# Optimization experiments

Hardware: AMD Instinct MI355X
Metric: run time of the kernel (lower is better)

## Reference

```python
import jax, jax.numpy as jnp
import numpy as np

BETA = 0.25
DECAY = 0.99
USAGE_DECAY = 0.99
EPS = 1e-5
RESET_THRESHOLD = 100.0


def _sqdist(x, e):
    # squared euclidean distances [N, K]; argmin identical to cdist argmin
    x2 = jnp.sum(x * x, axis=1, keepdims=True)           # [N,1]
    e2 = jnp.sum(e * e, axis=1)[None, :]                 # [1,K]
    return x2 - 2.0 * (x @ e.T) + e2


def setup_inputs() -> dict:
    key = jax.random.key(0)
    ks = jax.random.split(key, 7)
    N, K, D = 32768, 4096, 256
    return {
        "x": jax.random.normal(ks[0], (N, D), jnp.float32),
        "embedding": jax.random.normal(ks[1], (K, D), jnp.float32) * (1.0 / K),
        "ema_cluster_size": jax.random.uniform(ks[2], (K,), jnp.float32),
        "ema_w": jax.random.normal(ks[3], (K, D), jnp.float32) * (1.0 / K),
        "codebook_usage": jax.random.uniform(ks[4], (K,), jnp.float32),
        "steps_since_used": jax.random.randint(ks[5], (K,), 0, 200, jnp.int32),
        "random_indices": jax.random.randint(ks[6], (K,), 0, N, jnp.int32),
    }


def reference(x, embedding, ema_cluster_size, ema_w, codebook_usage,
              steps_since_used, random_indices):
    N, D = x.shape
    K = embedding.shape[0]

    # --- nearest-code lookup ---
    d2 = _sqdist(x, embedding)                 # [N,K]
    indices = jnp.argmin(d2, axis=1)           # [N]
    q = jnp.take(embedding, indices, axis=0)   # [N,D]
    quantized = x + jax.lax.stop_gradient(q - x)

    commitment_loss = jnp.mean((x - jax.lax.stop_gradient(quantized)) ** 2)
    loss = BETA * commitment_loss

    # --- EMA codebook update (encodings.sum(0) and encodings.T @ x as segment sums) ---
    counts = jax.ops.segment_sum(jnp.ones((N,), x.dtype), indices, num_segments=K)
    dw = jax.ops.segment_sum(x, indices, num_segments=K)        # [K,D]
    new_cs = ema_cluster_size * DECAY + (1.0 - DECAY) * counts
    new_ema_w = ema_w * DECAY + (1.0 - DECAY) * dw
    n = jnp.sum(new_cs)
    cluster_size = (new_cs + EPS) / (n + K * EPS) * n
    new_embedding = new_ema_w / cluster_size[:, None]
    new_usage = codebook_usage * USAGE_DECAY + (1.0 - USAGE_DECAY) * counts

    # --- dead-code reset (uses the EMA-updated codebook, as in the original) ---
    idx2 = jnp.argmin(_sqdist(x, new_embedding), axis=1)
    used = jax.ops.segment_sum(jnp.ones((N,), x.dtype), idx2, num_segments=K) > 0
    steps = jnp.where(used, 0.0, steps_since_used.astype(x.dtype) + 1.0)
    dead = steps > RESET_THRESHOLD
    replacement = jnp.take(x, random_indices, axis=0)           # [K,D]
    new_embedding = jnp.where(dead[:, None], replacement, new_embedding)
    steps = jnp.where(dead, 0.0, steps)

    usage_rate = jnp.mean((new_usage > 0).astype(x.dtype))

    return (quantized, indices, loss, new_embedding, new_cs, new_ema_w,
            new_usage, steps, usage_rate)
```

## Files before the change

### kernel.cpp

```cpp
#include <hip/hip_runtime.h>
#include <math.h>

typedef float vf4 __attribute__((ext_vector_type(4)));
typedef _Float16 f16;
typedef _Float16 f16x8 __attribute__((ext_vector_type(8)));
typedef _Float16 f16x4 __attribute__((ext_vector_type(4)));
typedef float f32x4 __attribute__((ext_vector_type(4)));

static constexpr int Ncnt = 32768;
static constexpr int Kcb  = 4096;
static constexpr int Dim  = 256;

static constexpr float EPSf  = 1e-5f;
static constexpr float KEPSf = (float)(4096.0 * 1e-5);

static constexpr size_t OQ  = 0;
static constexpr size_t OI  = (size_t)Ncnt * Dim;
static constexpr size_t OL  = OI + Ncnt;
static constexpr size_t OE  = OL + 1;
static constexpr size_t OCS = OE + (size_t)Kcb * Dim;
static constexpr size_t OW  = OCS + Kcb;
static constexpr size_t OU  = OW + (size_t)Kcb * Dim;
static constexpr size_t OS  = OU + Kcb;
static constexpr size_t OR  = OS + Kcb;

__device__ __forceinline__ float np_sq256(const float* __restrict__ p) {
  float tot[2];
  #pragma unroll
  for (int h = 0; h < 2; ++h) {
    const float* a = p + h * 128;
    float r[8];
    #pragma unroll
    for (int j = 0; j < 8; ++j) r[j] = __fmul_rn(a[j], a[j]);
    for (int i = 8; i < 128; i += 8)
      #pragma unroll
      for (int j = 0; j < 8; ++j) r[j] = __fadd_rn(r[j], __fmul_rn(a[i + j], a[i + j]));
    tot[h] = __fadd_rn(__fadd_rn(__fadd_rn(r[0], r[1]), __fadd_rn(r[2], r[3])),
                       __fadd_rn(__fadd_rn(r[4], r[5]), __fadd_rn(r[6], r[7])));
  }
  return __fadd_rn(tot[0], tot[1]);
}

__global__ void rowsq_np(const float* __restrict__ E, float* __restrict__ e2, int rows) {
  const int k = blockIdx.x * 256 + threadIdx.x;
  if (k < rows) e2[k] = np_sq256(E + (size_t)k * Dim);
}

__global__ void split_rows(const float* __restrict__ src, f16* __restrict__ dst,
                           const float scale, const int rows)
{
  const int i   = blockIdx.x * 256 + threadIdx.x;
  const int row = i >> 6;
  const int d0  = (i & 63) * 4;
  if (row >= rows) return;
  const vf4 v = *(const vf4*)(src + (size_t)row * 256 + d0);
  f16x4 hi, lo;
  #pragma unroll
  for (int j = 0; j < 4; ++j) {
    const float t = __fmul_rn(v[j], scale);
    const f16 h   = (f16)t;
    const float r = __fsub_rn(t, (float)h);
    hi[j] = h;
    lo[j] = (f16)r;
  }
  *(f16x4*)(dst + (size_t)row * 512 + d0)       = hi;
  *(f16x4*)(dst + (size_t)row * 512 + 256 + d0) = lo;
}

__global__ __launch_bounds__(256, 2) void mfma_argmin(
    const f16* __restrict__ Xs, const f16* __restrict__ Es,
    const float* __restrict__ e2, const float two_scale,
    int* __restrict__ cand)
{
  __shared__ __align__(16) f16 As[128 * 32];
  __shared__ __align__(16) f16 Bs[128 * 32];

  const int tid  = threadIdx.x;
  const int bid  = blockIdx.x;
  const int row0 = (bid >> 3) * 128;
  const int cg   = bid & 7;
  const int colbase = cg * 512;

  const int lane = tid & 63;
  const int wv   = tid >> 6;
  const int wr   = wv >> 1;
  const int wc   = wv & 1;
  const int lc   = lane & 15;
  const int kc   = lane >> 4;

  const int sr  = tid >> 1;
  const int sh  = tid & 1;
  const int ssw = (sr >> 1) & 3;
  f16* lA = As + sr * 32;
  f16* lB = Bs + sr * 32;
  const int w0 = ((2 * sh)     ^ ssw) * 8;
  const int w1 = ((2 * sh + 1) ^ ssw) * 8;

  const f16* aG = Xs + (size_t)(row0 + sr) * 512 + sh * 16;

  const int ks = (kc ^ ((lc >> 1) & 3)) * 8;

  float t1[16], t2[16];
  int   i1[16], i2[16];
  #pragma unroll
  for (int s = 0; s < 16; ++s) {
    t1[s] = INFINITY; t2[s] = INFINITY; i1[s] = 0x7fffffff; i2[s] = 0x7fffffff;
  }

  for (int ct = 0; ct < 4; ++ct) {
    const f16* bG = Es + (size_t)(colbase + ct * 128 + sr) * 512 + sh * 16;

    f32x4 acc[4][4];
    #pragma unroll
    for (int i = 0; i < 4; ++i)
      #pragma unroll
      for (int j = 0; j < 4; ++j)
        acc[i][j] = (f32x4){0.0f, 0.0f, 0.0f, 0.0f};

    f16x8 ra0 = *(const f16x8*)(aG);
    f16x8 ra1 = *(const f16x8*)(aG + 8);
    f16x8 rb0 = *(const f16x8*)(bG);
    f16x8 rb1 = *(const f16x8*)(bG + 8);

    for (int kk = 0; kk < 768; kk += 32) {
      *(f16x8*)(lA + w0) = ra0;
      *(f16x8*)(lA + w1) = ra1;
      *(f16x8*)(lB + w0) = rb0;
      *(f16x8*)(lB + w1) = rb1;
      __syncthreads();

      f16x8 af[4], bf[4];
      #pragma unroll
      for (int f = 0; f < 4; ++f) {
        af[f] = *(const f16x8*)(As + (wr * 64 + f * 16 + lc) * 32 + ks);
        bf[f] = *(const f16x8*)(Bs + (wc * 64 + f * 16 + lc) * 32 + ks);
      }

      if (kk + 32 < 768) {
        const int kn = kk + 32;
        const int aC = (kn < 512) ? kn : (kn - 512);
        const int bC = (kn < 256) ? kn : (kn - 256);
        ra0 = *(const f16x8*)(aG + aC);
        ra1 = *(const f16x8*)(aG + aC + 8);
        rb0 = *(const f16x8*)(bG + bC);
        rb1 = *(const f16x8*)(bG + bC + 8);
      }

      #pragma unroll
      for (int fm = 0; fm < 4; ++fm)
        #pragma unroll
        for (int fn = 0; fn < 4; ++fn)
          acc[fm][fn] = __builtin_amdgcn_mfma_f32_16x16x32_f16(
              af[fm], bf[fn], acc[fm][fn], 0, 0, 0);

      __syncthreads();
    }

    #pragma unroll
    for (int fm = 0; fm < 4; ++fm) {
      #pragma unroll
      for (int j = 0; j < 4; ++j) {
        const int s = fm * 4 + j;
        #pragma unroll
        for (int fn = 0; fn < 4; ++fn) {
          const int col = colbase + ct * 128 + wc * 64 + fn * 16 + lc;
          const float t = __fsub_rn(e2[col], __fmul_rn(two_scale, acc[fm][fn][j]));
          if (t < t1[s]) {
            t2[s] = t1[s]; i2[s] = i1[s]; t1[s] = t; i1[s] = col;
          } else if (t < t2[s]) {
            t2[s] = t; i2[s] = col;
          }
        }
      }
    }
  }

  #pragma unroll
  for (int s = 0; s < 16; ++s) {
    #pragma unroll
    for (int m = 1; m < 16; m <<= 1) {
      const float p1 = __shfl_xor(t1[s], m);
      const float p2 = __shfl_xor(t2[s], m);
      const int   q1 = __shfl_xor(i1[s], m);
      const int   q2 = __shfl_xor(i2[s], m);
      const bool pl = (p1 < t1[s]) || (p1 == t1[s] && q1 < i1[s]);
      float n1, n2; int m1, m2;
      if (pl) {
        n1 = p1; m1 = q1;
        const bool sl = (t1[s] < p2) || (t1[s] == p2 && i1[s] < q2);
        n2 = sl ? t1[s] : p2; m2 = sl ? i1[s] : q2;
      } else {
        n1 = t1[s]; m1 = i1[s];
        const bool sl = (p1 < t2[s]) || (p1 == t2[s] && q1 < i2[s]);
        n2 = sl ? p1 : t2[s]; m2 = sl ? q1 : i2[s];
      }
      t1[s] = n1; i1[s] = m1; t2[s] = n2; i2[s] = m2;
    }
  }

  if (lc == 0) {
    #pragma unroll
    for (int fm = 0; fm < 4; ++fm)
      #pragma unroll
      for (int j = 0; j < 4; ++j) {
        const int s    = fm * 4 + j;
        const int rloc = wr * 64 + fm * 16 + kc * 4 + j;
        const size_t base = ((size_t)(row0 + rloc) * 8 + cg) * 4 + wc * 2;
        cand[base]     = i1[s];
        cand[base + 1] = i2[s];
      }
  }
}

__global__ void recheck(const float* __restrict__ X, const float* __restrict__ x2g,
                        const float* __restrict__ Eref, const float* __restrict__ e2ref,
                        const int* __restrict__ cand, int* __restrict__ idxo)
{
  __shared__ float Xl[8][256];
  const int tid  = threadIdx.x;
  const int rg   = tid >> 5;
  const int lr   = tid & 31;
  const int row0 = blockIdx.x * 8;
  const int row  = row0 + rg;

  {
    const float* xp = X + (size_t)row * 256 + lr * 8;
    *(vf4*)(&Xl[rg][lr * 8])     = *(const vf4*)xp;
    *(vf4*)(&Xl[rg][lr * 8 + 4]) = *(const vf4*)(xp + 4);
  }
  __syncthreads();

  int k = cand[(size_t)row * 32 + lr];

  float acc = 0.0f;
  const float* ep = Eref + (size_t)k * 256;
  for (int d4 = 0; d4 < 64; ++d4) {
    const vf4 xv = *(const vf4*)(&Xl[rg][d4 * 4]);
    const vf4 ev = *(const vf4*)(ep + d4 * 4);
    acc = fmaf(xv[0], ev[0], acc);
    acc = fmaf(xv[1], ev[1], acc);
    acc = fmaf(xv[2], ev[2], acc);
    acc = fmaf(xv[3], ev[3], acc);
  }
  float s = __fadd_rn(__fsub_rn(x2g[row], __fmul_rn(2.0f, acc)), e2ref[k]);

  #pragma unroll
  for (int m = 1; m < 32; m <<= 1) {
    const float os = __shfl_xor(s, m);
    const int   ok = __shfl_xor(k, m);
    if (os < s || (os == s && ok < k)) { s = os; k = ok; }
  }
  if (lr == 0) idxo[row] = k;
}

__global__ void stats_cd(const float* __restrict__ X, const float* __restrict__ E,
                         const int* __restrict__ idx, float* __restrict__ counts,
                         float* __restrict__ dw, double* __restrict__ loss_acc)
{
  __shared__ double part[4];
  const int tid  = threadIdx.x;
  const int lane = tid & 63, w = tid >> 6;
  const int row  = blockIdx.x * 4 + w;
  const int k    = idx[row];
  const vf4 xv = ((const vf4*)X)[(size_t)row * 64 + lane];
  const vf4 qv = ((const vf4*)E)[(size_t)k * 64 + lane];
  const float d0 = xv[0]-qv[0], d1 = xv[1]-qv[1], d2 = xv[2]-qv[2], d3 = xv[3]-qv[3];
  double ps = (double)(d0*d0 + d1*d1 + d2*d2 + d3*d3);
  #pragma unroll
  for (int o = 32; o; o >>= 1) ps += __shfl_down(ps, o);
  #pragma unroll
  for (int j = 0; j < 4; ++j)
    atomicAdd(dw + (size_t)k * Dim + lane * 4 + j, xv[j]);
  if (lane == 0) {
    part[w] = ps;
    atomicAdd(counts + k, 1.0f);
  }
  __syncthreads();
  if (tid == 0) atomicAdd(loss_acc, part[0] + part[1] + part[2] + part[3]);
}

__global__ void gather_q(const float* __restrict__ E, const int* __restrict__ idx,
                         float* __restrict__ out)
{
  const int tid  = threadIdx.x;
  const int lane = tid & 63, w = tid >> 6;
  const int row  = blockIdx.x * 4 + w;
  const int k    = idx[row];
  ((vf4*)out)[(size_t)row * 64 + lane] = ((const vf4*)E)[(size_t)k * 64 + lane];
  if (lane == 0) out[OI + row] = (float)k;
}

__global__ void cs_usage(const float* __restrict__ ecs, const float* __restrict__ usage,
                         const float* __restrict__ counts, float* __restrict__ out,
                         int* __restrict__ pos_cnt)
{
  __shared__ int si[256];
  const int tid = threadIdx.x;
  const int k   = blockIdx.x * 256 + tid;
  const float cnt = counts[k];
  const float ncs = __fadd_rn(__fmul_rn(ecs[k], 0.99f), __fmul_rn(0.01f, cnt));
  out[OCS + k] = ncs;
  const float nus = __fadd_rn(__fmul_rn(usage[k], 0.99f), __fmul_rn(0.01f, cnt));
  out[OU + k] = nus;
  si[tid] = (nus > 0.0f) ? 1 : 0;
  __syncthreads();
  for (int s = 128; s; s >>= 1) {
    if (tid < s) si[tid] += si[tid + s];
    __syncthreads();
  }
  if (tid == 0) atomicAdd(pos_cnt, si[0]);
}

__global__ void n_np_kernel(const float* __restrict__ ncs, float* __restrict__ nf) {
  __shared__ float leaf[32];
  const int t = threadIdx.x;
  if (t < 32) {
    const float* a = ncs + t * 128;
    float r[8];
    #pragma unroll
    for (int j = 0; j < 8; ++j) r[j] = a[j];
    for (int i = 8; i < 128; i += 8)
      #pragma unroll
      for (int j = 0; j < 8; ++j) r[j] = __fadd_rn(r[j], a[i + j]);
    leaf[t] = __fadd_rn(__fadd_rn(__fadd_rn(r[0], r[1]), __fadd_rn(r[2], r[3])),
                        __fadd_rn(__fadd_rn(r[4], r[5]), __fadd_rn(r[6], r[7])));
  }
  __syncthreads();
  if (t == 0) {
    float v[32];
    #pragma unroll
    for (int i = 0; i < 32; ++i) v[i] = leaf[i];
    for (int n = 32; n > 1; n >>= 1)
      for (int i = 0; i < (n >> 1); ++i) v[i] = __fadd_rn(v[2 * i], v[2 * i + 1]);
    *nf = v[0];
  }
}

__global__ void emb_pre(const float* __restrict__ emaw, float* __restrict__ out,
                        const float* __restrict__ nf)
{
  const int k = blockIdx.x;
  const int d = threadIdx.x;
  const size_t o = (size_t)k * Dim + d;
  const float dwv = out[OW + o];
  const float w = __fadd_rn(__fmul_rn(emaw[o], 0.99f), __fmul_rn(0.01f, dwv));
  out[OW + o] = w;
  const float nv  = *nf;
  const float ncs = out[OCS + k];
  const float cs  = __fmul_rn(__fdiv_rn(__fadd_rn(ncs, EPSf), __fadd_rn(nv, KEPSf)), nv);
  out[OE + o] = __fdiv_rn(w, cs);
}

__global__ void used_scatter(const int* __restrict__ idx2, int* __restrict__ used) {
  const int i = blockIdx.x * 256 + threadIdx.x;
  used[idx2[i]] = 1;
}

__global__ void finalize_k(const float* __restrict__ X, const int* __restrict__ used,
                           const int* __restrict__ steps_in, const int* __restrict__ rnd,
                           float* __restrict__ out)
{
  const int k = blockIdx.x, d = threadIdx.x;
  const int u = used[k];
  const float st = u ? 0.0f : (float)steps_in[k] + 1.0f;
  const bool dead = st > 100.0f;
  if (dead) out[OE + (size_t)k * Dim + d] = X[(size_t)rnd[k] * Dim + d];
  if (d == 0) out[OS + k] = dead ? 0.0f : st;
}

__global__ void write_scalars(const double* __restrict__ loss_acc,
                              const int* __restrict__ pos_cnt, float* __restrict__ out)
{
  if (threadIdx.x == 0) {
    out[OL] = 0.25f * (float)(*loss_acc / (double)((size_t)Ncnt * Dim));
    out[OR] = (float)(*pos_cnt) / (float)Kcb;
  }
}

extern "C" void kernel_launch(void* const* d_in, const int* in_sizes, int n_in,
                              void* d_out, int out_size, void* d_ws, size_t ws_size,
                              hipStream_t stream)
{
  const float* X     = (const float*)d_in[0];
  const float* E     = (const float*)d_in[1];
  const float* ECS   = (const float*)d_in[2];
  const float* EMAW  = (const float*)d_in[3];
  const float* USAGE = (const float*)d_in[4];
  const int*   STEPS = (const int*)d_in[5];
  const int*   RND   = (const int*)d_in[6];
  float* out = (float*)d_out;

  float* wsf = (float*)d_ws;
  float*  counts   = wsf;
  int*    used     = (int*)(wsf + 4096);
  double* loss_acc = (double*)(wsf + 8192);
  float*  nf       = wsf + 8194;
  int*    pos_cnt  = (int*)(wsf + 8195);
  const size_t ZN  = 8200;
  float* x2g  = wsf + 8320;
  float* e2   = wsf + 41088;
  float* e2p  = wsf + 45184;
  int*   idx1 = (int*)(wsf + 49280);
  int*   idx2 = (int*)(wsf + 82048);
  f16*   Es   = (f16*)(wsf + 114816);
  int*   cand = (int*)(wsf + 1163392);
  f16*   Xsp  = (f16*)out;

  hipMemsetAsync(d_ws, 0, ZN * sizeof(float), stream);
  hipMemsetAsync(out + OW, 0, (size_t)Kcb * Dim * sizeof(float), stream);

  rowsq_np     <<<Ncnt / 256, 256, 0, stream>>>(X, x2g, Ncnt);
  rowsq_np     <<<Kcb / 256,  256, 0, stream>>>(E, e2, Kcb);
  split_rows   <<<Ncnt / 4,   256, 0, stream>>>(X, Xsp, 64.0f, Ncnt);
  split_rows   <<<Kcb / 4,    256, 0, stream>>>(E, Es, 16777216.0f, Kcb);
  mfma_argmin  <<<2048,       256, 0, stream>>>(Xsp, Es, e2, 0x1p-29f, cand);
  recheck      <<<Ncnt / 8,   256, 0, stream>>>(X, x2g, E, e2, cand, idx1);
  stats_cd     <<<Ncnt / 4,   256, 0, stream>>>(X, E, idx1, counts, out + OW, loss_acc);
  cs_usage     <<<Kcb / 256,  256, 0, stream>>>(ECS, USAGE, counts, out, pos_cnt);
  n_np_kernel  <<<1,          64,  0, stream>>>(out + OCS, nf);
  emb_pre      <<<Kcb,        256, 0, stream>>>(EMAW, out, nf);
  rowsq_np     <<<Kcb / 256,  256, 0, stream>>>(out + OE, e2p, Kcb);
  split_rows   <<<Kcb / 4,    256, 0, stream>>>(out + OE, Es, 256.0f, Kcb);
  mfma_argmin  <<<2048,       256, 0, stream>>>(Xsp, Es, e2p, 0x1p-13f, cand);
  recheck      <<<Ncnt / 8,   256, 0, stream>>>(X, x2g, out + OE, e2p, cand, idx2);
  used_scatter <<<Ncnt / 256, 256, 0, stream>>>(idx2, used);
  finalize_k   <<<Kcb,        256, 0, stream>>>(X, used, STEPS, RND, out);
  gather_q     <<<Ncnt / 4,   256, 0, stream>>>(E, idx1, out);
  write_scalars<<<1,          64,  0, stream>>>(loss_acc, pos_cnt, out);

  (void)in_sizes; (void)n_in; (void)out_size; (void)ws_size;
}
```

Measured before the change: 1.908 ms.

## Load GEMM tiles directly into LDS with global_load_lds in argmin kernel

Replaces the register-staged global-to-LDS copy in the MFMA argmin kernel with direct global_load_lds transfers, with a new per-wave row mapping and XOR chunk swizzle. The K loop is fully unrolled and issues the next tile's load right after the fragment reads. e2 values are hoisted once per column tile, and the distance term now uses a single fmaf instead of a separately rounded multiply and subtract. This is meant to cut VGPR use and copy instructions, at the cost of no double buffering, and the fused rounding may change argmin ties.

```diff
diff --git a/kernel.cpp b/kernel.cpp
--- a/kernel.cpp
+++ b/kernel.cpp
@@ -24,6 +24,11 @@
 static constexpr size_t OS  = OU + Kcb;
 static constexpr size_t OR  = OS + Kcb;
 
+#define GLD16(gp, lp)                                                   \
+  __builtin_amdgcn_global_load_lds(                                     \
+      (const __attribute__((address_space(1))) void*)(gp),              \
+      (__attribute__((address_space(3))) void*)(lp), 16, 0, 0)
+
 __device__ __forceinline__ float np_sq256(const float* __restrict__ p) {
   float tot[2];
   #pragma unroll
@@ -81,24 +86,27 @@
   const int cg   = bid & 7;
   const int colbase = cg * 512;
 
-  const int lane = tid & 63;
-  const int wv   = tid >> 6;
-  const int wr   = wv >> 1;
-  const int wc   = wv & 1;
-  const int lc   = lane & 15;
-  const int kc   = lane >> 4;
-
-  const int sr  = tid >> 1;
-  const int sh  = tid & 1;
-  const int ssw = (sr >> 1) & 3;
-  f16* lA = As + sr * 32;
-  f16* lB = Bs + sr * 32;
-  const int w0 = ((2 * sh)     ^ ssw) * 8;
-  const int w1 = ((2 * sh + 1) ^ ssw) * 8;
-
-  const f16* aG = Xs + (size_t)(row0 + sr) * 512 + sh * 16;
+  const int l  = tid & 63;
+  const int wv = tid >> 6;
+  const int wr = wv >> 1;
+  const int wc = wv & 1;
+  const int lc = l & 15;
+  const int kc = l >> 4;
+
+  const int srow = wv * 32 + (l >> 2);
+  const int chs  = (l & 3) ^ ((l >> 3) & 3);
+
+  const f16* aB0 = Xs + (size_t)(row0 + srow) * 512 + chs * 8;
+  const f16* aB1 = aB0 + 16 * 512;
+
+  f16* lA0 = As + wv * 1024;
+  f16* lA1 = As + wv * 1024 + 512;
+  f16* lB0 = Bs + wv * 1024;
+  f16* lB1 = Bs + wv * 1024 + 512;
 
   const int ks = (kc ^ ((lc >> 1) & 3)) * 8;
+
+  const float nts = -two_scale;
 
   float t1[16], t2[16];
   int   i1[16], i2[16];
@@ -107,8 +115,10 @@
     t1[s] = INFINITY; t2[s] = INFINITY; i1[s] = 0x7fffffff; i2[s] = 0x7fffffff;
   }
 
+  #pragma unroll 1
   for (int ct = 0; ct < 4; ++ct) {
-    const f16* bG = Es + (size_t)(colbase + ct * 128 + sr) * 512 + sh * 16;
+    const f16* bB0 = Es + (size_t)(colbase + ct * 128 + srow) * 512 + chs * 8;
+    const f16* bB1 = bB0 + 16 * 512;
 
     f32x4 acc[4][4];
     #pragma unroll
@@ -117,16 +127,11 @@
       for (int j = 0; j < 4; ++j)
         acc[i][j] = (f32x4){0.0f, 0.0f, 0.0f, 0.0f};
 
-    f16x8 ra0 = *(const f16x8*)(aG);
-    f16x8 ra1 = *(const f16x8*)(aG + 8);
-    f16x8 rb0 = *(const f16x8*)(bG);
-    f16x8 rb1 = *(const f16x8*)(bG + 8);
-
-    for (int kk = 0; kk < 768; kk += 32) {
-      *(f16x8*)(lA + w0) = ra0;
-      *(f16x8*)(lA + w1) = ra1;
-      *(f16x8*)(lB + w0) = rb0;
-      *(f16x8*)(lB + w1) = rb1;
+    GLD16(aB0, lA0); GLD16(aB1, lA1);
+    GLD16(bB0, lB0); GLD16(bB1, lB1);
+
+    #pragma unroll
+    for (int st = 0; st < 24; ++st) {
       __syncthreads();
 
       f16x8 af[4], bf[4];
@@ -135,15 +140,14 @@
         af[f] = *(const f16x8*)(As + (wr * 64 + f * 16 + lc) * 32 + ks);
         bf[f] = *(const f16x8*)(Bs + (wc * 64 + f * 16 + lc) * 32 + ks);
       }
-
-      if (kk + 32 < 768) {
-        const int kn = kk + 32;
-        const int aC = (kn < 512) ? kn : (kn - 512);
-        const int bC = (kn < 256) ? kn : (kn - 256);
-        ra0 = *(const f16x8*)(aG + aC);
-        ra1 = *(const f16x8*)(aG + aC + 8);
-        rb0 = *(const f16x8*)(bG + bC);
-        rb1 = *(const f16x8*)(bG + bC + 8);
+      __syncthreads();
+
+      if (st + 1 < 24) {
+        const int sn = st + 1;
+        const int aO = ((sn >> 3) == 1 ? 256 : 0) + (sn & 7) * 32;
+        const int bO = ((sn >> 3) == 0 ? 0 : 256) + (sn & 7) * 32;
+        GLD16(aB0 + aO, lA0); GLD16(aB1 + aO, lA1);
+        GLD16(bB0 + bO, lB0); GLD16(bB1 + bO, lB1);
       }
 
       #pragma unroll
@@ -152,9 +156,12 @@
         for (int fn = 0; fn < 4; ++fn)
           acc[fm][fn] = __builtin_amdgcn_mfma_f32_16x16x32_f16(
               af[fm], bf[fn], acc[fm][fn], 0, 0, 0);
-
-      __syncthreads();
     }
+
+    float e2v[4];
+    #pragma unroll
+    for (int fn = 0; fn < 4; ++fn)
+      e2v[fn] = e2[colbase + ct * 128 + wc * 64 + fn * 16 + lc];
 
     #pragma unroll
     for (int fm = 0; fm < 4; ++fm) {
@@ -164,7 +171,7 @@
         #pragma unroll
         for (int fn = 0; fn < 4; ++fn) {
           const int col = colbase + ct * 128 + wc * 64 + fn * 16 + lc;
-          const float t = __fsub_rn(e2[col], __fmul_rn(two_scale, acc[fm][fn][j]));
+          const float t = fmaf(nts, acc[fm][fn][j], e2v[fn]);
           if (t < t1[s]) {
             t2[s] = t1[s]; i2[s] = i1[s]; t1[s] = t; i1[s] = col;
           } else if (t < t2[s]) {
```

After: 1.915 ms. No clear change (+0.3%).
